# Performance work log

Measured on AMD Instinct MI355X. Metric: run time of the kernel, lower is better.

## Reference

```python
import jax, jax.numpy as jnp
import numpy as np

B, T, E, H = 8, 512, 64, 128
ALPHA, ETA, THETA = 0.999, 0.95, 0.05
BETA = 1.0 - ALPHA


def _l2norm_axis1(a):
    # torch F.normalize default: p=2, dim=1, eps=1e-12
    n = jnp.linalg.norm(a, axis=1, keepdims=True)
    return a / jnp.maximum(n, 1e-12)


def _mlp(W1, b1, W2, b2, x):
    # x: (B, E); per-batch-element MLP (ParallelMLPs)
    h = jax.nn.silu(jnp.einsum('bhe,be->bh', W1, x) + b1)  # (B, H)
    return jnp.einsum('beh,bh->be', W2, h) + b2            # (B, E)


def setup_inputs():
    key = jax.random.key(0)
    ks = jax.random.split(key, 5)
    x = jax.random.normal(ks[0], (B, T, E), jnp.float32)
    lim = float(np.sqrt(6.0 / (E + E)))  # xavier_uniform for K/V weights
    WK = jax.random.uniform(ks[1], (E, E), jnp.float32, -lim, lim)
    WV = jax.random.uniform(ks[2], (E, E), jnp.float32, -lim, lim)
    W1 = 0.02 * jax.random.normal(ks[3], (B, H, E), jnp.float32)  # template init std=0.02
    b1 = jnp.zeros((B, H), jnp.float32)
    W2 = 0.02 * jax.random.normal(ks[4], (B, E, H), jnp.float32)
    b2 = jnp.zeros((B, E), jnp.float32)
    SW1 = jnp.zeros((B, H, E), jnp.float32)
    Sb1 = jnp.zeros((B, H), jnp.float32)
    SW2 = jnp.zeros((B, E, H), jnp.float32)
    Sb2 = jnp.zeros((B, E), jnp.float32)
    return {"x": x, "WK": WK, "WV": WV, "W1": W1, "b1": b1, "W2": W2,
            "b2": b2, "SW1": SW1, "Sb1": Sb1, "SW2": SW2, "Sb2": Sb2}


def reference(x, WK, WV, W1, b1, W2, b2, SW1, Sb1, SW2, Sb2):
    # keys / values: Linear (no bias) -> SiLU -> L2-normalize along dim=1 (torch default)
    keys = _l2norm_axis1(jax.nn.silu(x @ WK.T))    # (B, T, E)
    values = _l2norm_axis1(jax.nn.silu(x @ WV.T))  # (B, T, E)
    kT = jnp.transpose(keys, (1, 0, 2))            # (T, B, E)
    vT = jnp.transpose(values, (1, 0, 2))

    def loss_fn(params, k, v):
        y = _mlp(*params, k)
        return jnp.mean((y - v) ** 2)

    # per-token grads & losses: vmap(grad_and_value) over the sequence dim
    losses, grads = jax.vmap(jax.value_and_grad(loss_fn), in_axes=(None, 0, 0))(
        (W1, b1, W2, b2), kT, vT)  # losses (T,), grads[i] (T, *param_shape)

    beta_vec = jnp.full((T,), BETA, jnp.float32)
    eta_vec = jnp.full((T,), ETA, jnp.float32)
    theta_vec = jnp.full((T,), THETA, jnp.float32)

    p_prefix = jnp.cumprod(beta_vec)
    p_suffix = jnp.cumprod(beta_vec[::-1])[::-1]
    q_prefix = jnp.cumprod(eta_vec)
    q_suffix = jnp.cumprod(eta_vec[::-1])[::-1]
    p_T = p_prefix[-1]
    q_T = q_prefix[-1]
    w = p_suffix / beta_vec * q_prefix
    A_T = w.sum()
    partial_sum = jnp.cumsum(w[::-1])[::-1]
    B_coeffs = -theta_vec * partial_sum / q_prefix
    D_coeffs = -theta_vec * q_suffix

    def upd(g, M0, S0):
        gB = jnp.tensordot(B_coeffs, g, axes=(0, 0))  # sum_t B[t] * g[t]
        gD = jnp.tensordot(D_coeffs, g, axes=(0, 0))
        return p_T * M0 + A_T * S0 + gB, q_T * S0 + gD

    new_state = [upd(g, M0, S0) for g, M0, S0 in
                 zip(grads, (W1, b1, W2, b2), (SW1, Sb1, SW2, Sb2))]
    parts = [losses] + [m.ravel() for m, _ in new_state] + [s.ravel() for _, s in new_state]
    return jnp.concatenate(parts)
```

## Files before the change

### kernel.cpp

```cpp
#include <hip/hip_runtime.h>
#include <math.h>

#define NB 8
#define NT 512
#define NE 64
#define NH 128

#define WS_K    0
#define WS_V    262144
#define WS_IVK  524288
#define WS_IVV  524800
#define WS_H    525312
#define WS_DY   1049600
#define WS_DZ   1311744
#define WS_LP   1836032

#define O_LOSS  0
#define O_MW1   512
#define O_MB1   66048
#define O_MW2   67072
#define O_MB2   132608
#define O_SW1   133120
#define O_SB1   198656
#define O_SW2   199680
#define O_SB2   265216

#define POISON_F (-3.0316488252093987e-13f)

__device__ __forceinline__ float bcast(float v, int lane) {
    return __uint_as_float(__builtin_amdgcn_readlane(__float_as_uint(v), (unsigned)lane));
}

__device__ __forceinline__ float silu_f(float x) {
    return x / (1.f + expf(-x));
}

__global__ __launch_bounds__(256) void k_kv(const float* __restrict__ x,
                                            const float* __restrict__ WK,
                                            const float* __restrict__ WV,
                                            float* __restrict__ ws) {
    __shared__ float sWK[64 * 65];
    __shared__ float sWV[64 * 65];
    __shared__ float rK[256], rV[256];
    int tid = threadIdx.x;
    for (int i = tid; i < 4096; i += 256) {
        int e = i >> 6, j = i & 63;
        sWK[e * 65 + j] = WK[i];
        sWV[e * 65 + j] = WV[i];
    }
    __syncthreads();
    int idx = blockIdx.x * 256 + tid;
    int row = idx >> 6, e = idx & 63;
    const float4* xr4 = (const float4*)(x + row * 64);
    float ak = 0.f, av = 0.f;
#pragma unroll
    for (int j4 = 0; j4 < 16; ++j4) {
        float4 xv = xr4[j4];
        const float* wk = &sWK[e * 65 + j4 * 4];
        const float* wv = &sWV[e * 65 + j4 * 4];
        ak += xv.x * wk[0] + xv.y * wk[1] + xv.z * wk[2] + xv.w * wk[3];
        av += xv.x * wv[0] + xv.y * wv[1] + xv.z * wv[2] + xv.w * wv[3];
    }
    float kk = silu_f(ak), vv = silu_f(av);
    ws[WS_K + idx] = kk;
    ws[WS_V + idx] = vv;
    rK[tid] = kk * kk;
    rV[tid] = vv * vv;
    __syncthreads();
    int b = blockIdx.x >> 7;
    if (tid < 64) {
        atomicAdd(&ws[WS_IVK + b * 64 + tid],
                  rK[tid] + rK[tid + 64] + rK[tid + 128] + rK[tid + 192]);
    } else if (tid < 128) {
        int l = tid & 63;
        atomicAdd(&ws[WS_IVV + b * 64 + l],
                  rV[l] + rV[l + 64] + rV[l + 128] + rV[l + 192]);
    }
}

__global__ __launch_bounds__(256) void k_fwdbwd(const float* __restrict__ W1,
                                               const float* __restrict__ b1,
                                               const float* __restrict__ W2,
                                               const float* __restrict__ b2,
                                               float* __restrict__ ws) {
    __shared__ float sW1[NE * NH];
    __shared__ float sW2[NE * NH];
    int tid = threadIdx.x;
    int b = blockIdx.x >> 6;
    int chunk = blockIdx.x & 63;
    int w = tid >> 6, l = tid & 63;

    const float4* W14 = (const float4*)(W1 + b * 8192);
    const float4* W24 = (const float4*)(W2 + b * 8192);
#pragma unroll
    for (int k4 = 0; k4 < 8; ++k4) {
        int i4 = tid + k4 * 256;
        float4 a = W14[i4];
        int i = i4 * 4;
        int hh = i >> 6, eb = i & 63;
        sW1[(eb + 0) * 128 + (hh ^ ((eb + 0) & 31))] = a.x;
        sW1[(eb + 1) * 128 + (hh ^ ((eb + 1) & 31))] = a.y;
        sW1[(eb + 2) * 128 + (hh ^ ((eb + 2) & 31))] = a.z;
        sW1[(eb + 3) * 128 + (hh ^ ((eb + 3) & 31))] = a.w;
        float4 c = W24[i4];
        int ee = i >> 7, hb = i & 127, sw = ee & 31;
        sW2[ee * 128 + ((hb + 0) ^ sw)] = c.x;
        sW2[ee * 128 + ((hb + 1) ^ sw)] = c.y;
        sW2[ee * 128 + ((hb + 2) ^ sw)] = c.z;
        sW2[ee * 128 + ((hb + 3) ^ sw)] = c.w;
    }
    __syncthreads();

    float ivK = 1.f / fmaxf(sqrtf(ws[WS_IVK + b * 64 + l] - POISON_F), 1e-12f);
    float ivV = 1.f / fmaxf(sqrtf(ws[WS_IVV + b * 64 + l] - POISON_F), 1e-12f);
    float b1lo = b1[b * 128 + l], b1hi = b1[b * 128 + 64 + l];
    float b2l = b2[b * 64 + l];
    int t0 = chunk * 8 + w * 2;

    int rowE[2], rowH[2];
    float kv[2], vv[2];
#pragma unroll
    for (int j = 0; j < 2; ++j) {
        int t = t0 + j;
        rowE[j] = (b * NT + t) * NE;
        rowH[j] = (b * NT + t) * NH;
        kv[j] = ws[WS_K + rowE[j] + l] * ivK;
        vv[j] = ws[WS_V + rowE[j] + l] * ivV;
    }

    float zlo[2], zhi[2];
#pragma unroll
    for (int j = 0; j < 2; ++j) { zlo[j] = b1lo; zhi[j] = b1hi; }
    for (int e = 0; e < 64; ++e) {
        int sw = e & 31;
        float w0 = sW1[e * 128 + (l ^ sw)];
        float w1 = sW1[e * 128 + (l ^ sw) + 64];
#pragma unroll
        for (int j = 0; j < 2; ++j) {
            float kk = bcast(kv[j], e);
            zlo[j] += w0 * kk;
            zhi[j] += w1 * kk;
        }
    }
    float hlo[2], hhi[2];
#pragma unroll
    for (int j = 0; j < 2; ++j) { hlo[j] = silu_f(zlo[j]); hhi[j] = silu_f(zhi[j]); }

    float y[2];
#pragma unroll
    for (int j = 0; j < 2; ++j) y[j] = b2l;
    {
        int sw2 = l & 31;
        for (int hh = 0; hh < 64; ++hh) {
            float w0 = sW2[l * 128 + (hh ^ sw2)];
            float w1 = sW2[l * 128 + (hh ^ sw2) + 64];
#pragma unroll
            for (int j = 0; j < 2; ++j) {
                y[j] += w0 * bcast(hlo[j], hh) + w1 * bcast(hhi[j], hh);
            }
        }
    }

    float dyv[2], lp[2];
#pragma unroll
    for (int j = 0; j < 2; ++j) {
        float d = y[j] - vv[j];
        dyv[j] = d * (2.f / 512.f);
        lp[j] = d * d;
    }
#pragma unroll
    for (int m = 32; m; m >>= 1) {
#pragma unroll
        for (int j = 0; j < 2; ++j) lp[j] += __shfl_xor(lp[j], m);
    }
    if (l == 0) {
#pragma unroll
        for (int j = 0; j < 2; ++j) ws[WS_LP + b * NT + t0 + j] = lp[j];
    }

    float dhlo[2] = {0.f, 0.f}, dhhi[2] = {0.f, 0.f};
    for (int e = 0; e < 64; ++e) {
        int sw = e & 31;
        float w0 = sW2[e * 128 + (l ^ sw)];
        float w1 = sW2[e * 128 + (l ^ sw) + 64];
#pragma unroll
        for (int j = 0; j < 2; ++j) {
            float dd = bcast(dyv[j], e);
            dhlo[j] += w0 * dd;
            dhhi[j] += w1 * dd;
        }
    }

#pragma unroll
    for (int j = 0; j < 2; ++j) {
        float slo = 1.f / (1.f + expf(-zlo[j]));
        float shi = 1.f / (1.f + expf(-zhi[j]));
        float dz0 = dhlo[j] * (slo * (1.f + zlo[j] * (1.f - slo)));
        float dz1 = dhhi[j] * (shi * (1.f + zhi[j] * (1.f - shi)));
        ws[WS_DZ + rowH[j] + l] = dz0;
        ws[WS_DZ + rowH[j] + 64 + l] = dz1;
        ws[WS_H + rowH[j] + l] = hlo[j];
        ws[WS_H + rowH[j] + 64 + l] = hhi[j];
        ws[WS_DY + rowE[j] + l] = dyv[j];
        ws[WS_K + rowE[j] + l] = kv[j];
    }
}

__global__ __launch_bounds__(1024) void k_state(const float* __restrict__ ws,
                                                const float* __restrict__ W1,
                                                const float* __restrict__ b1,
                                                const float* __restrict__ W2,
                                                const float* __restrict__ b2,
                                                const float* __restrict__ SW1,
                                                const float* __restrict__ Sb1,
                                                const float* __restrict__ SW2,
                                                const float* __restrict__ Sb2,
                                                float* __restrict__ out) {
    __shared__ float sBC[512], sDC[512], sSC[3];
    __shared__ float sM[1024], sS[1024], sMb[16], sSb[16];
    int bi = blockIdx.x, tid = threadIdx.x;

    if (bi == 512) {
        if (tid < 512) {
            float s = 0.f;
#pragma unroll
            for (int b = 0; b < NB; ++b) s += ws[WS_LP + b * NT + tid];
            out[O_LOSS + tid] = s * (1.f / 512.f);
        }
        return;
    }

    const float L2ETA = -0.07400058144f;
    const float L2R   = -9.89178369f;
    const float INV1MR = 1.0f / (1.0f - 0.001052631579f);
    if (tid < 512) {
        float ePow = exp2f((float)(511 - tid) * L2ETA);
        float rPow = exp2f((float)(512 - tid) * L2R);
        sBC[tid] = -0.05f * ePow * (1.f - rPow) * INV1MR;
        sDC[tid] = -0.05f * 0.95f * ePow;
    } else if (tid == 512) {
        float q = exp2f(512.f * L2ETA);
        sSC[0] = 0.f;
        sSC[1] = q * INV1MR;
        sSC[2] = q;
    }
    __syncthreads();

    int tg = tid >> 8;
    int t0 = tg * 128;
    float accM = 0.f, accS = 0.f, accMb = 0.f, accSb = 0.f;

    if (bi < 256) {
        int b = bi >> 5, hb = (bi & 31) << 2;
        int hidx = (tid >> 6) & 3, e = tid & 63;
        int h = hb + hidx;
        const float* kb = ws + WS_K + b * NT * NE + e;
        const float* dzb = ws + WS_DZ + b * NT * NH + h;
#pragma unroll 8
        for (int t = t0; t < t0 + 128; ++t) {
            float kvt = kb[t * NE];
            float dzt = dzb[t * NH];
            float gb = sBC[t] * dzt, gd = sDC[t] * dzt;
            accM += gb * kvt; accS += gd * kvt;
            accMb += gb;      accSb += gd;
        }
        sM[tid] = accM; sS[tid] = accS;
        if (e == 0) { sMb[tg * 4 + hidx] = accMb; sSb[tg * 4 + hidx] = accSb; }
        __syncthreads();
        float pT = sSC[0], AT = sSC[1], qT = sSC[2];
        if (tid < 256) {
            float m = sM[tid] + sM[tid + 256] + sM[tid + 512] + sM[tid + 768];
            float s = sS[tid] + sS[tid + 256] + sS[tid + 512] + sS[tid + 768];
            int idx = (b * NH + h) * NE + e;
            out[O_MW1 + idx] = pT * W1[idx] + AT * SW1[idx] + m;
            out[O_SW1 + idx] = qT * SW1[idx] + s;
        }
        if (tid < 4) {
            float mb = sMb[tid] + sMb[4 + tid] + sMb[8 + tid] + sMb[12 + tid];
            float sb = sSb[tid] + sSb[4 + tid] + sSb[8 + tid] + sSb[12 + tid];
            int ib = b * NH + hb + tid;
            out[O_MB1 + ib] = pT * b1[ib] + AT * Sb1[ib] + mb;
            out[O_SB1 + ib] = qT * Sb1[ib] + sb;
        }
    } else {
        int bi2 = bi - 256;
        int b = bi2 >> 5, eb = (bi2 & 31) << 1;
        int eidx = (tid >> 7) & 1, h = tid & 127;
        int e = eb + eidx;
        const float* dyb = ws + WS_DY + b * NT * NE + e;
        const float* hbuf = ws + WS_H + b * NT * NH + h;
#pragma unroll 8
        for (int t = t0; t < t0 + 128; ++t) {
            float dyt = dyb[t * NE];
            float hht = hbuf[t * NH];
            float gb = sBC[t] * dyt, gd = sDC[t] * dyt;
            accM += gb * hht; accS += gd * hht;
            accMb += gb;      accSb += gd;
        }
        sM[tid] = accM; sS[tid] = accS;
        if (h == 0) { sMb[tg * 4 + eidx] = accMb; sSb[tg * 4 + eidx] = accSb; }
        __syncthreads();
        float pT = sSC[0], AT = sSC[1], qT = sSC[2];
        if (tid < 256) {
            float m = sM[tid] + sM[tid + 256] + sM[tid + 512] + sM[tid + 768];
            float s = sS[tid] + sS[tid + 256] + sS[tid + 512] + sS[tid + 768];
            int idx = (b * NE + e) * NH + h;
            out[O_MW2 + idx] = pT * W2[idx] + AT * SW2[idx] + m;
            out[O_SW2 + idx] = qT * SW2[idx] + s;
        }
        if (tid < 2) {
            float mb = sMb[tid] + sMb[4 + tid] + sMb[8 + tid] + sMb[12 + tid];
            float sb = sSb[tid] + sSb[4 + tid] + sSb[8 + tid] + sSb[12 + tid];
            int ib = b * NE + eb + tid;
            out[O_MB2 + ib] = pT * b2[ib] + AT * Sb2[ib] + mb;
            out[O_SB2 + ib] = qT * Sb2[ib] + sb;
        }
    }
}

extern "C" void kernel_launch(void* const* d_in, const int* in_sizes, int n_in,
                              void* d_out, int out_size, void* d_ws, size_t ws_size,
                              hipStream_t stream) {
    const float* x   = (const float*)d_in[0];
    const float* WK  = (const float*)d_in[1];
    const float* WV  = (const float*)d_in[2];
    const float* W1  = (const float*)d_in[3];
    const float* b1  = (const float*)d_in[4];
    const float* W2  = (const float*)d_in[5];
    const float* b2  = (const float*)d_in[6];
    const float* SW1 = (const float*)d_in[7];
    const float* Sb1 = (const float*)d_in[8];
    const float* SW2 = (const float*)d_in[9];
    const float* Sb2 = (const float*)d_in[10];
    float* out = (float*)d_out;
    float* ws = (float*)d_ws;

    hipLaunchKernelGGL(k_kv,     dim3(1024), dim3(256),  0, stream, x, WK, WV, ws);
    hipLaunchKernelGGL(k_fwdbwd, dim3(512),  dim3(256),  0, stream, W1, b1, W2, b2, ws);
    hipLaunchKernelGGL(k_state,  dim3(513),  dim3(1024), 0, stream,
                       ws, W1, b1, W2, b2, SW1, Sb1, SW2, Sb2, out);
}
```

Baseline: 115.8 us.

## Vectorize state-update reduction with float4 per-thread tiles and defer key normalization

k_state now runs 256-thread blocks in which each thread accumulates four output columns. It reads the key and hidden rows as float4, which gives more reuse of each dz/dy load and more coalesced loads. The forward/backward kernel no longer writes normalized keys. Instead, the per-column inverse norm is applied once to the reduced W1 sums, using the sum-of-squares buffer from the key/value kernel. The p_T*M0 term is dropped because p_T underflows to zero. The change relies on the workspace K and IVK buffers holding the expected unnormalized data and poison offset.

```diff
diff --git a/kernel.cpp b/kernel.cpp
--- a/kernel.cpp
+++ b/kernel.cpp
@@ -202,118 +202,153 @@
         ws[WS_H + rowH[j] + l] = hlo[j];
         ws[WS_H + rowH[j] + 64 + l] = hhi[j];
         ws[WS_DY + rowE[j] + l] = dyv[j];
-        ws[WS_K + rowE[j] + l] = kv[j];
-    }
-}
-
-__global__ __launch_bounds__(1024) void k_state(const float* __restrict__ ws,
-                                                const float* __restrict__ W1,
-                                                const float* __restrict__ b1,
-                                                const float* __restrict__ W2,
-                                                const float* __restrict__ b2,
-                                                const float* __restrict__ SW1,
-                                                const float* __restrict__ Sb1,
-                                                const float* __restrict__ SW2,
-                                                const float* __restrict__ Sb2,
-                                                float* __restrict__ out) {
-    __shared__ float sBC[512], sDC[512], sSC[3];
-    __shared__ float sM[1024], sS[1024], sMb[16], sSb[16];
+    }
+}
+
+__global__ __launch_bounds__(256) void k_state(const float* __restrict__ ws,
+                                               const float* __restrict__ W1,
+                                               const float* __restrict__ b1,
+                                               const float* __restrict__ W2,
+                                               const float* __restrict__ b2,
+                                               const float* __restrict__ SW1,
+                                               const float* __restrict__ Sb1,
+                                               const float* __restrict__ SW2,
+                                               const float* __restrict__ Sb2,
+                                               float* __restrict__ out) {
     int bi = blockIdx.x, tid = threadIdx.x;
 
     if (bi == 512) {
-        if (tid < 512) {
+#pragma unroll
+        for (int r = 0; r < 2; ++r) {
+            int t = tid + r * 256;
             float s = 0.f;
 #pragma unroll
-            for (int b = 0; b < NB; ++b) s += ws[WS_LP + b * NT + tid];
-            out[O_LOSS + tid] = s * (1.f / 512.f);
+            for (int b = 0; b < NB; ++b) s += ws[WS_LP + b * NT + t];
+            out[O_LOSS + t] = s * (1.f / 512.f);
         }
         return;
     }
+
+    __shared__ float sBC[512], sDC[512];
+    __shared__ float sRed[10][256];
 
     const float L2ETA = -0.07400058144f;
     const float L2R   = -9.89178369f;
     const float INV1MR = 1.0f / (1.0f - 0.001052631579f);
-    if (tid < 512) {
-        float ePow = exp2f((float)(511 - tid) * L2ETA);
-        float rPow = exp2f((float)(512 - tid) * L2R);
-        sBC[tid] = -0.05f * ePow * (1.f - rPow) * INV1MR;
-        sDC[tid] = -0.05f * 0.95f * ePow;
-    } else if (tid == 512) {
-        float q = exp2f(512.f * L2ETA);
-        sSC[0] = 0.f;
-        sSC[1] = q * INV1MR;
-        sSC[2] = q;
-    }
-    __syncthreads();
-
-    int tg = tid >> 8;
-    int t0 = tg * 128;
-    float accM = 0.f, accS = 0.f, accMb = 0.f, accSb = 0.f;
+#pragma unroll
+    for (int r = 0; r < 2; ++r) {
+        int t = tid + r * 256;
+        float ePow = exp2f((float)(511 - t) * L2ETA);
+        float rPow = exp2f((float)(512 - t) * L2R);
+        sBC[t] = -0.05f * ePow * (1.f - rPow) * INV1MR;
+        sDC[t] = -0.05f * 0.95f * ePow;
+    }
+    __syncthreads();
+
+    int chunk = tid >> 6, job = tid & 63;
+    int t0 = chunk * 128;
+    float4 accM = {0.f, 0.f, 0.f, 0.f}, accS = {0.f, 0.f, 0.f, 0.f};
+    float accMb = 0.f, accSb = 0.f;
 
     if (bi < 256) {
-        int b = bi >> 5, hb = (bi & 31) << 2;
-        int hidx = (tid >> 6) & 3, e = tid & 63;
-        int h = hb + hidx;
-        const float* kb = ws + WS_K + b * NT * NE + e;
+        int b = bi >> 5;
+        int h = ((bi & 31) << 2) + (job >> 4), eq = job & 15;
+        const float4* kq = (const float4*)(ws + WS_K + b * NT * NE) + eq;
         const float* dzb = ws + WS_DZ + b * NT * NH + h;
-#pragma unroll 8
+#pragma unroll 4
         for (int t = t0; t < t0 + 128; ++t) {
-            float kvt = kb[t * NE];
-            float dzt = dzb[t * NH];
+            float4 k4 = kq[t * 16];
+            float dzt = dzb[t * 128];
             float gb = sBC[t] * dzt, gd = sDC[t] * dzt;
-            accM += gb * kvt; accS += gd * kvt;
-            accMb += gb;      accSb += gd;
-        }
-        sM[tid] = accM; sS[tid] = accS;
-        if (e == 0) { sMb[tg * 4 + hidx] = accMb; sSb[tg * 4 + hidx] = accSb; }
-        __syncthreads();
-        float pT = sSC[0], AT = sSC[1], qT = sSC[2];
-        if (tid < 256) {
-            float m = sM[tid] + sM[tid + 256] + sM[tid + 512] + sM[tid + 768];
-            float s = sS[tid] + sS[tid + 256] + sS[tid + 512] + sS[tid + 768];
-            int idx = (b * NH + h) * NE + e;
-            out[O_MW1 + idx] = pT * W1[idx] + AT * SW1[idx] + m;
-            out[O_SW1 + idx] = qT * SW1[idx] + s;
-        }
-        if (tid < 4) {
-            float mb = sMb[tid] + sMb[4 + tid] + sMb[8 + tid] + sMb[12 + tid];
-            float sb = sSb[tid] + sSb[4 + tid] + sSb[8 + tid] + sSb[12 + tid];
-            int ib = b * NH + hb + tid;
-            out[O_MB1 + ib] = pT * b1[ib] + AT * Sb1[ib] + mb;
-            out[O_SB1 + ib] = qT * Sb1[ib] + sb;
+            accM.x += gb * k4.x; accM.y += gb * k4.y;
+            accM.z += gb * k4.z; accM.w += gb * k4.w;
+            accS.x += gd * k4.x; accS.y += gd * k4.y;
+            accS.z += gd * k4.z; accS.w += gd * k4.w;
+            accMb += gb; accSb += gd;
         }
     } else {
-        int bi2 = bi - 256;
-        int b = bi2 >> 5, eb = (bi2 & 31) << 1;
-        int eidx = (tid >> 7) & 1, h = tid & 127;
-        int e = eb + eidx;
+        int bj = bi - 256;
+        int b = bj >> 5;
+        int e = ((bj & 31) << 1) + (job >> 5), hq = job & 31;
+        const float4* hp = (const float4*)(ws + WS_H + b * NT * NH) + hq;
         const float* dyb = ws + WS_DY + b * NT * NE + e;
-        const float* hbuf = ws + WS_H + b * NT * NH + h;
-#pragma unroll 8
+#pragma unroll 4
         for (int t = t0; t < t0 + 128; ++t) {
-            float dyt = dyb[t * NE];
-            float hht = hbuf[t * NH];
+            float4 h4 = hp[t * 32];
+            float dyt = dyb[t * 64];
             float gb = sBC[t] * dyt, gd = sDC[t] * dyt;
-            accM += gb * hht; accS += gd * hht;
-            accMb += gb;      accSb += gd;
-        }
-        sM[tid] = accM; sS[tid] = accS;
-        if (h == 0) { sMb[tg * 4 + eidx] = accMb; sSb[tg * 4 + eidx] = accSb; }
-        __syncthreads();
-        float pT = sSC[0], AT = sSC[1], qT = sSC[2];
-        if (tid < 256) {
-            float m = sM[tid] + sM[tid + 256] + sM[tid + 512] + sM[tid + 768];
-            float s = sS[tid] + sS[tid + 256] + sS[tid + 512] + sS[tid + 768];
-            int idx = (b * NE + e) * NH + h;
-            out[O_MW2 + idx] = pT * W2[idx] + AT * SW2[idx] + m;
-            out[O_SW2 + idx] = qT * SW2[idx] + s;
-        }
-        if (tid < 2) {
-            float mb = sMb[tid] + sMb[4 + tid] + sMb[8 + tid] + sMb[12 + tid];
-            float sb = sSb[tid] + sSb[4 + tid] + sSb[8 + tid] + sSb[12 + tid];
-            int ib = b * NE + eb + tid;
-            out[O_MB2 + ib] = pT * b2[ib] + AT * Sb2[ib] + mb;
-            out[O_SB2 + ib] = qT * Sb2[ib] + sb;
+            accM.x += gb * h4.x; accM.y += gb * h4.y;
+            accM.z += gb * h4.z; accM.w += gb * h4.w;
+            accS.x += gd * h4.x; accS.y += gd * h4.y;
+            accS.z += gd * h4.z; accS.w += gd * h4.w;
+            accMb += gb; accSb += gd;
+        }
+    }
+
+    sRed[0][tid] = accM.x; sRed[1][tid] = accM.y;
+    sRed[2][tid] = accM.z; sRed[3][tid] = accM.w;
+    sRed[4][tid] = accS.x; sRed[5][tid] = accS.y;
+    sRed[6][tid] = accS.z; sRed[7][tid] = accS.w;
+    sRed[8][tid] = accMb;  sRed[9][tid] = accSb;
+    __syncthreads();
+    if (tid >= 64) return;
+
+    float v[10];
+#pragma unroll
+    for (int r = 0; r < 10; ++r)
+        v[r] = sRed[r][tid] + sRed[r][tid + 64] + sRed[r][tid + 128] + sRed[r][tid + 192];
+
+    float qT = exp2f(512.f * L2ETA);
+    float AT = qT * INV1MR;
+
+    if (bi < 256) {
+        int b = bi >> 5;
+        int h = ((bi & 31) << 2) + (tid >> 4), eq = tid & 15;
+        float4 ss = ((const float4*)(ws + WS_IVK + b * 64))[eq];
+        float4 iv;
+        iv.x = 1.f / fmaxf(sqrtf(ss.x - POISON_F), 1e-12f);
+        iv.y = 1.f / fmaxf(sqrtf(ss.y - POISON_F), 1e-12f);
+        iv.z = 1.f / fmaxf(sqrtf(ss.z - POISON_F), 1e-12f);
+        iv.w = 1.f / fmaxf(sqrtf(ss.w - POISON_F), 1e-12f);
+        int idx = (b * NH + h) * NE + (eq << 2);
+        float4 sw1 = *(const float4*)(SW1 + idx);
+        float4 om, os;
+        om.x = AT * sw1.x + v[0] * iv.x;
+        om.y = AT * sw1.y + v[1] * iv.y;
+        om.z = AT * sw1.z + v[2] * iv.z;
+        om.w = AT * sw1.w + v[3] * iv.w;
+        os.x = qT * sw1.x + v[4] * iv.x;
+        os.y = qT * sw1.y + v[5] * iv.y;
+        os.z = qT * sw1.z + v[6] * iv.z;
+        os.w = qT * sw1.w + v[7] * iv.w;
+        *(float4*)(out + O_MW1 + idx) = om;
+        *(float4*)(out + O_SW1 + idx) = os;
+        if (eq == 0) {
+            int ib = b * NH + h;
+            out[O_MB1 + ib] = AT * Sb1[ib] + v[8];
+            out[O_SB1 + ib] = qT * Sb1[ib] + v[9];
+        }
+    } else {
+        int bj = bi - 256;
+        int b = bj >> 5;
+        int e = ((bj & 31) << 1) + (tid >> 5), hq = tid & 31;
+        int idx = (b * NE + e) * NH + (hq << 2);
+        float4 sw2 = *(const float4*)(SW2 + idx);
+        float4 om, os;
+        om.x = AT * sw2.x + v[0];
+        om.y = AT * sw2.y + v[1];
+        om.z = AT * sw2.z + v[2];
+        om.w = AT * sw2.w + v[3];
+        os.x = qT * sw2.x + v[4];
+        os.y = qT * sw2.y + v[5];
+        os.z = qT * sw2.z + v[6];
+        os.w = qT * sw2.w + v[7];
+        *(float4*)(out + O_MW2 + idx) = om;
+        *(float4*)(out + O_SW2 + idx) = os;
+        if (hq == 0) {
+            int ib = b * NE + e;
+            out[O_MB2 + ib] = AT * Sb2[ib] + v[8];
+            out[O_SB2 + ib] = qT * Sb2[ib] + v[9];
         }
     }
 }
@@ -335,8 +370,8 @@
     float* out = (float*)d_out;
     float* ws = (float*)d_ws;
 
-    hipLaunchKernelGGL(k_kv,     dim3(1024), dim3(256),  0, stream, x, WK, WV, ws);
-    hipLaunchKernelGGL(k_fwdbwd, dim3(512),  dim3(256),  0, stream, W1, b1, W2, b2, ws);
-    hipLaunchKernelGGL(k_state,  dim3(513),  dim3(1024), 0, stream,
+    hipLaunchKernelGGL(k_kv,     dim3(1024), dim3(256), 0, stream, x, WK, WV, ws);
+    hipLaunchKernelGGL(k_fwdbwd, dim3(512),  dim3(256), 0, stream, W1, b1, W2, b2, ws);
+    hipLaunchKernelGGL(k_state,  dim3(513),  dim3(256), 0, stream,
                        ws, W1, b1, W2, b2, SW1, Sb1, SW2, Sb2, out);
 }
```

Measured after the change: 114.5 us. About the same (-1.1%).
